# Performance work log

Measured on AMD Instinct MI355X. Metric: run time of the kernel, lower is better.

Reference implementation:

```python
import jax, jax.numpy as jnp
import numpy as np
from functools import partial

K_NEIGHBOURS = 16
POS_SLICE = (0, 2)  # pos_indices = slice(0, 2)


def setup_inputs() -> dict:
    key = jax.random.key(0)
    ks = jax.random.split(key, 8)
    B, A, D, H = 512, 128, 32, 128
    obs = jax.random.normal(ks[0], (B, A, D), dtype=jnp.float32)
    # GCNConv params (glorot-ish scale) and output MLP
    W1 = jax.random.normal(ks[1], (D, H), dtype=jnp.float32) / np.sqrt(D)
    b1 = jnp.zeros((H,), dtype=jnp.float32)
    W2 = jax.random.normal(ks[2], (H, H), dtype=jnp.float32) / np.sqrt(H)
    b2 = jnp.zeros((H,), dtype=jnp.float32)
    Wout = jax.random.normal(ks[3], (H, 1), dtype=jnp.float32) / np.sqrt(H)
    bout = jnp.zeros((1,), dtype=jnp.float32)
    return {"agent_observations": obs, "W1": W1, "b1": b1, "W2": W2, "b2": b2,
            "Wout": Wout, "bout": bout}


def _build_knn_edges(obs):
    """Vectorized kNN graph construction (replaces per-batch python loop).
    Returns (row, col) of shape [B*A*k] with batch offsets applied.
    row = source node i, col = j-th nearest neighbour of i (self excluded)."""
    B, A, _ = obs.shape
    k = K_NEIGHBOURS
    pos = obs[:, :, POS_SLICE[0]:POS_SLICE[1]]  # [B, A, 2]
    diff = pos[:, :, None, :] - pos[:, None, :, :]  # [B, A, A, 2]
    dist = jnp.sqrt(jnp.sum(diff * diff, axis=-1))  # [B, A, A] (cdist p=2)
    # k+1 smallest distances (self at distance 0 is dropped)
    _, knn_idx = jax.lax.top_k(-dist, k + 1)  # [B, A, k+1]
    neighbor_idx = knn_idx[..., 1:]  # [B, A, k]
    offsets = (jnp.arange(B, dtype=jnp.int32) * A)[:, None, None]
    src = jnp.broadcast_to(jnp.arange(A, dtype=jnp.int32)[None, :, None], (B, A, k)) + offsets
    dst = neighbor_idx.astype(jnp.int32) + offsets
    return src.reshape(-1), dst.reshape(-1)


def _gcn_conv(x, row, col, deg_inv_sqrt, W, b, num_nodes):
    """PyG GCNConv: self-loops + symmetric normalization.
    out[c] = sum_{(r,c) in E} d[r]*d[c]*(xW)[r] + d[c]^2*(xW)[c] + b"""
    h = x @ W  # [N, H]
    norm = deg_inv_sqrt[row] * deg_inv_sqrt[col]  # [E]
    agg = jax.ops.segment_sum(norm[:, None] * h[row], col, num_segments=num_nodes)
    self_term = (deg_inv_sqrt * deg_inv_sqrt)[:, None] * h  # self-loop messages
    return agg + self_term + b


def reference(agent_observations, W1, b1, W2, b2, Wout, bout):
    obs = agent_observations.astype(jnp.float32)
    B, A, D = obs.shape
    N = B * A
    row, col = _build_knn_edges(obs)
    x = obs.reshape(N, D)
    # degree with self-loop weight 1 (PyG gcn_norm): deg[c] = 1 + in-degree(c)
    deg = 1.0 + jax.ops.segment_sum(jnp.ones_like(col, dtype=x.dtype), col, num_segments=N)
    deg_inv_sqrt = jax.lax.rsqrt(deg)
    x = jnp.tanh(_gcn_conv(x, row, col, deg_inv_sqrt, W1, b1, N))
    x = jnp.tanh(_gcn_conv(x, row, col, deg_inv_sqrt, W2, b2, N))
    out = x @ Wout + bout  # [N, 1]
    return out.reshape(B, A, 1)
```

## Files before the change

kernel.cpp:

```cpp
#include <hip/hip_runtime.h>

#define NA 128
#define NKN 16

typedef _Float16 f16;
typedef __fp16   h16x2 __attribute__((ext_vector_type(2)));
typedef _Float16 f16x8 __attribute__((ext_vector_type(8)));
typedef float    f32x16 __attribute__((ext_vector_type(16)));
typedef unsigned long long u64;

#define MFMA __builtin_amdgcn_mfma_f32_32x32x16_f16
#define SWZ16(row, byteoff) ((byteoff) ^ (((row)&15)<<4))
#define SWZ4(row, byteoff)  ((byteoff) ^ (((row)&3)<<4))
#define CSW(ia, l) ((l) ^ (((ia) & 15) << 1))

__device__ __forceinline__ float tanh_fast(float x){
    float e = __expf(2.f * x);
    return 1.f - 2.f * __builtin_amdgcn_rcpf(e + 1.f);
}

__device__ __forceinline__ unsigned int wsel(const uint4 c, int i){
    return i==0 ? c.x : i==1 ? c.y : i==2 ? c.z : c.w;
}

__device__ __forceinline__ void agg_mm(const unsigned char* matIn, unsigned char* matOut,
                                       const unsigned int (*cmask)[4], const float* dinv_s,
                                       const float* bias, const u64* lut,
                                       int wv, int lane)
{
    const int lr = lane & 31, lg = lane >> 5;
    const int rb = wv & 3, ch = wv >> 2;
    f32x16 c0, c1;
    #pragma unroll
    for (int e = 0; e < 16; ++e) { c0[e] = 0.f; c1[e] = 0.f; }

    const int j0 = ch*64 + lr, j1 = j0 + 32;
    const uint4 cm0 = *(const uint4*)&cmask[j0][0];
    const uint4 cm1 = *(const uint4*)&cmask[j1][0];
    const int row = rb*32 + lr;

    #pragma unroll
    for (int ks = 0; ks < 8; ++ks) {
        f16x8 af = *(const f16x8*)(matIn + row*256 + SWZ16(row, ks*32 + lg*16));
        const int sh = (ks&1)*16 + lg*8;
        const unsigned int b0 = (wsel(cm0, ks>>1) >> sh) & 0xFFu;
        const unsigned int b1 = (wsel(cm1, ks>>1) >> sh) & 0xFFu;
        union { f16x8 v; u64 u[2]; } B0, B1;
        B0.u[0] = lut[b0 & 15u]; B0.u[1] = lut[b0 >> 4];
        B1.u[0] = lut[b1 & 15u]; B1.u[1] = lut[b1 >> 4];
        c0 = MFMA(af, B0.v, c0, 0, 0, 0);
        c1 = MFMA(af, B1.v, c1, 0, 0, 0);
    }
    #pragma unroll
    for (int ct = 0; ct < 2; ++ct) {
        const int j = ct ? j1 : j0;
        const float dj = dinv_s[j];
        #pragma unroll
        for (int q = 0; q < 4; ++q) {
            const int r0 = rb*32 + q*8 + lg*4;
            const float4 bv = *(const float4*)&bias[r0];
            float v0, v1, v2, v3;
            if (ct == 0) {
                v0 = tanh_fast(fmaf(dj, c0[q*4+0], bv.x));
                v1 = tanh_fast(fmaf(dj, c0[q*4+1], bv.y));
                v2 = tanh_fast(fmaf(dj, c0[q*4+2], bv.z));
                v3 = tanh_fast(fmaf(dj, c0[q*4+3], bv.w));
            } else {
                v0 = tanh_fast(fmaf(dj, c1[q*4+0], bv.x));
                v1 = tanh_fast(fmaf(dj, c1[q*4+1], bv.y));
                v2 = tanh_fast(fmaf(dj, c1[q*4+2], bv.z));
                v3 = tanh_fast(fmaf(dj, c1[q*4+3], bv.w));
            }
            union { h16x2 h[2]; u64 u; } pk;
            pk.h[0] = __builtin_amdgcn_cvt_pkrtz(v0, v1);
            pk.h[1] = __builtin_amdgcn_cvt_pkrtz(v2, v3);
            *(u64*)(matOut + j*256 + SWZ16(j, r0*2)) = pk.u;
        }
    }
}

__global__ __launch_bounds__(512, 1) void prep(const float* __restrict__ W1g,
                                               const float* __restrict__ W2g,
                                               unsigned char* __restrict__ ws)
{
    const int m = blockIdx.x * 512 + threadIdx.x;
    if (m < 2048) {
        const int h2 = m & 127, g = m >> 7;
        f16x8 v;
        #pragma unroll
        for (int s = 0; s < 8; ++s) v[s] = (f16)W2g[(g*8 + s)*128 + h2];
        *(f16x8*)(ws + 8192 + h2*256 + SWZ16(h2, g*16)) = v;
    } else {
        const int m2 = m - 2048;
        const int h = m2 & 127, g = m2 >> 7;
        f16x8 v;
        #pragma unroll
        for (int s = 0; s < 8; ++s) v[s] = (f16)W1g[(g*8 + s)*128 + h];
        *(f16x8*)(ws + h*64 + SWZ4(h, g*16)) = v;
    }
}

__global__ __launch_bounds__(512, 4) void gnn_fused(
    const float* __restrict__ obs,
    const unsigned char* __restrict__ ws,
    const float* __restrict__ b1g, const float* __restrict__ b2g,
    const float* __restrict__ Wog, const float* __restrict__ bog,
    float* __restrict__ outg)
{
    __shared__ __align__(16) unsigned char mat0[32768];
    __shared__ __align__(16) unsigned char mat1[32768];
    __shared__ float posx[NA], posy[NA], dinv_s[NA], b1s[NA], b2s[NA], wos[NA];
    __shared__ unsigned int cmask[NA][4];
    __shared__ unsigned int ccnt[NA];
    __shared__ u64 lut16[16];

    const int t = threadIdx.x;
    const int b = blockIdx.x;
    const int wv = t >> 6, lane = t & 63;
    const int lr = lane & 31, lg = lane >> 5;

    {
        const float4* ob = (const float4*)(obs + (size_t)b * NA * 32);
        #pragma unroll
        for (int rep = 0; rep < 2; ++rep) {
            const int idx = rep*512 + t;
            const int i = idx >> 3, seg = idx & 7;
            const float4 v = ob[idx];
            if (seg == 0) { posx[i] = v.x; posy[i] = v.y; }
            union { h16x2 h[2]; u64 u; } pk;
            pk.h[0] = __builtin_amdgcn_cvt_pkrtz(v.x, v.y);
            pk.h[1] = __builtin_amdgcn_cvt_pkrtz(v.z, v.w);
            *(u64*)(mat1 + i*64 + SWZ4(i, seg*8)) = pk.u;
        }
        u64* cand = (u64*)mat0;
        #pragma unroll
        for (int s = 0; s < 8; ++s) cand[t*8 + s] = ~0ull;
        if (t < NA) { b1s[t] = b1g[t]; b2s[t] = b2g[t]; wos[t] = Wog[t]; ccnt[t] = 0u; }
        { const int j = t >> 2, w = t & 3; cmask[j][w] = (w == (j>>5)) ? (1u << (j&31)) : 0u; }
        if (t < 16) {
            u64 e = 0ull;
            #pragma unroll
            for (int s = 0; s < 4; ++s)
                if ((t >> s) & 1) e |= 0x3C00ull << (16*s);
            lut16[t] = e;
        }
    }
    __syncthreads();

    const int ia = t >> 2, p4 = t & 3;
    {
        u64* cand = (u64*)mat0;
        unsigned int kd[32];
        const float xi = posx[ia], yi = posy[ia];
        #pragma unroll
        for (int jj = 0; jj < 32; ++jj) {
            const int j = p4*32 + jj;
            const float dx = __fsub_rn(xi, posx[j]);
            const float dy = __fsub_rn(yi, posy[j]);
            const float d  = __fsqrt_rn(__fadd_rn(__fmul_rn(dx,dx), __fmul_rn(dy,dy)));
            kd[jj] = __float_as_uint(d);
        }
        unsigned int lo = 0u, hi = 0xFF000000u, P = 0u;
        bool done = false;
        #pragma unroll 1
        for (int it = 0; it < 34; ++it) {
            const unsigned int mid = (lo + hi) >> 1;
            int cl = 0;
            #pragma unroll
            for (int jj = 0; jj < 32; ++jj) cl += (kd[jj] < mid) ? 1 : 0;
            cl += __shfl_xor(cl, 1, 64);
            cl += __shfl_xor(cl, 2, 64);
            if (!done) {
                if (cl >= 17 && cl <= 32) { P = mid; done = true; }
                else if (cl < 17) lo = mid;
                else hi = mid;
                if (hi - lo <= 1u && !done) { P = hi; done = true; }
            }
            if (__all(done ? 1 : 0)) break;
        }
        if (!done) P = hi;
        #pragma unroll
        for (int jj = 0; jj < 32; ++jj) {
            if (kd[jj] < P) {
                const unsigned int s = atomicAdd(&ccnt[ia], 1u);
                if (s < 32u)
                    cand[ia*32 + CSW(ia, s)] = ((u64)kd[jj] << 32) | (unsigned)(p4*32 + jj);
            }
        }
    }
    __syncthreads();
    {
        const u64* cand = (const u64*)mat0;
        u64 ck8[8];
        int rk[8];
        #pragma unroll
        for (int q = 0; q < 8; ++q) {
            ck8[q] = cand[ia*32 + CSW(ia, 8*p4 + q)];
            rk[q] = 0;
        }
        #pragma unroll
        for (int e = 0; e < 32; ++e) {
            const u64 ke = cand[ia*32 + CSW(ia, e)];
            #pragma unroll
            for (int q = 0; q < 8; ++q) rk[q] += (ke < ck8[q]) ? 1 : 0;
        }
        const int m = (int)min(ccnt[ia], 32u);
        #pragma unroll
        for (int q = 0; q < 8; ++q) {
            const int c = 8*p4 + q;
            if (c < m && rk[q] >= 1 && rk[q] < 17) {
                const int n = (int)(ck8[q] & 127u);
                atomicOr(&cmask[n][ia >> 5], 1u << (ia & 31));
            }
        }
    }
    __syncthreads();
    if (t < NA)
        dinv_s[t] = rsqrtf((float)(__popc(cmask[t][0]) + __popc(cmask[t][1]) +
                                   __popc(cmask[t][2]) + __popc(cmask[t][3])));
    *(f16x8*)(mat0 + t*16) = *(const f16x8*)(ws + t*16);
    __syncthreads();

    {
        f32x16 c0, c1;
        #pragma unroll
        for (int e = 0; e < 16; ++e) { c0[e] = 0.f; c1[e] = 0.f; }
        const int rb = wv & 3, ch = wv >> 2;
        const int row = rb*32 + lr;
        #pragma unroll
        for (int ks = 0; ks < 2; ++ks) {
            const f16x8 af = *(const f16x8*)(mat1 + row*64 + SWZ4(row, ks*32 + lg*16));
            #pragma unroll
            for (int ct = 0; ct < 2; ++ct) {
                const int h = ch*64 + ct*32 + lr;
                const f16x8 bf = *(const f16x8*)(mat0 + h*64 + SWZ4(h, ks*32 + lg*16));
                if (ct == 0) c0 = MFMA(af, bf, c0, 0, 0, 0);
                else         c1 = MFMA(af, bf, c1, 0, 0, 0);
            }
        }
        __syncthreads();
        #pragma unroll
        for (int ct = 0; ct < 2; ++ct) {
            const int h = ch*64 + ct*32 + lr;
            #pragma unroll
            for (int q = 0; q < 4; ++q) {
                const int r0 = rb*32 + q*8 + lg*4;
                const float4 dv = *(const float4*)&dinv_s[r0];
                union { h16x2 hh[2]; u64 u; } pk;
                if (ct == 0) {
                    pk.hh[0] = __builtin_amdgcn_cvt_pkrtz(c0[q*4+0]*dv.x, c0[q*4+1]*dv.y);
                    pk.hh[1] = __builtin_amdgcn_cvt_pkrtz(c0[q*4+2]*dv.z, c0[q*4+3]*dv.w);
                } else {
                    pk.hh[0] = __builtin_amdgcn_cvt_pkrtz(c1[q*4+0]*dv.x, c1[q*4+1]*dv.y);
                    pk.hh[1] = __builtin_amdgcn_cvt_pkrtz(c1[q*4+2]*dv.z, c1[q*4+3]*dv.w);
                }
                *(u64*)(mat0 + h*256 + SWZ16(h, r0*2)) = pk.u;
            }
        }
    }
    __syncthreads();

    agg_mm(mat0, mat1, cmask, dinv_s, b1s, lut16, wv, lane);
    __syncthreads();

    {
        #pragma unroll
        for (int rep = 0; rep < 4; ++rep) {
            const int idx = rep*512 + t;
            *(f16x8*)(mat0 + idx*16) = *(const f16x8*)(ws + 8192 + idx*16);
        }
    }
    __syncthreads();
    {
        f32x16 c0, c1;
        #pragma unroll
        for (int e = 0; e < 16; ++e) { c0[e] = 0.f; c1[e] = 0.f; }
        const int rb = wv & 3, ch = wv >> 2;
        const int row = rb*32 + lr;
        #pragma unroll
        for (int ks = 0; ks < 8; ++ks) {
            const f16x8 af = *(const f16x8*)(mat1 + row*256 + SWZ16(row, ks*32 + lg*16));
            #pragma unroll
            for (int ct = 0; ct < 2; ++ct) {
                const int h2 = ch*64 + ct*32 + lr;
                const f16x8 bf = *(const f16x8*)(mat0 + h2*256 + SWZ16(h2, ks*32 + lg*16));
                if (ct == 0) c0 = MFMA(af, bf, c0, 0, 0, 0);
                else         c1 = MFMA(af, bf, c1, 0, 0, 0);
            }
        }
        __syncthreads();
        #pragma unroll
        for (int ct = 0; ct < 2; ++ct) {
            const int h2 = ch*64 + ct*32 + lr;
            #pragma unroll
            for (int q = 0; q < 4; ++q) {
                const int r0 = rb*32 + q*8 + lg*4;
                const float4 dv = *(const float4*)&dinv_s[r0];
                union { h16x2 hh[2]; u64 u; } pk;
                if (ct == 0) {
                    pk.hh[0] = __builtin_amdgcn_cvt_pkrtz(c0[q*4+0]*dv.x, c0[q*4+1]*dv.y);
                    pk.hh[1] = __builtin_amdgcn_cvt_pkrtz(c0[q*4+2]*dv.z, c0[q*4+3]*dv.w);
                } else {
                    pk.hh[0] = __builtin_amdgcn_cvt_pkrtz(c1[q*4+0]*dv.x, c1[q*4+1]*dv.y);
                    pk.hh[1] = __builtin_amdgcn_cvt_pkrtz(c1[q*4+2]*dv.z, c1[q*4+3]*dv.w);
                }
                *(u64*)(mat1 + h2*256 + SWZ16(h2, r0*2)) = pk.u;
            }
        }
    }
    __syncthreads();

    agg_mm(mat1, mat0, cmask, dinv_s, b2s, lut16, wv, lane);
    __syncthreads();

    {
        float s = 0.f;
        #pragma unroll
        for (int u = 0; u < 4; ++u) {
            const f16x8 v = *(const f16x8*)(mat0 + ia*256 + SWZ16(ia, p4*64 + u*16));
            const float4 w0 = *(const float4*)&wos[p4*32 + u*8];
            const float4 w1 = *(const float4*)&wos[p4*32 + u*8 + 4];
            s = fmaf((float)v[0], w0.x, s); s = fmaf((float)v[1], w0.y, s);
            s = fmaf((float)v[2], w0.z, s); s = fmaf((float)v[3], w0.w, s);
            s = fmaf((float)v[4], w1.x, s); s = fmaf((float)v[5], w1.y, s);
            s = fmaf((float)v[6], w1.z, s); s = fmaf((float)v[7], w1.w, s);
        }
        s += __shfl_xor(s, 1, 64);
        s += __shfl_xor(s, 2, 64);
        if (p4 == 0) outg[b*NA + ia] = s + bog[0];
    }
}

extern "C" void kernel_launch(void* const* d_in, const int* in_sizes, int n_in,
                              void* d_out, int out_size, void* d_ws, size_t ws_size,
                              hipStream_t stream) {
    const float* obs = (const float*)d_in[0];
    const float* W1  = (const float*)d_in[1];
    const float* b1  = (const float*)d_in[2];
    const float* W2  = (const float*)d_in[3];
    const float* b2  = (const float*)d_in[4];
    const float* Wo  = (const float*)d_in[5];
    const float* bo  = (const float*)d_in[6];
    float* out = (float*)d_out;
    const int B = in_sizes[0] / (NA * 32);
    unsigned char* ws = (unsigned char*)d_ws;
    hipLaunchKernelGGL(prep, dim3(5), dim3(512), 0, stream, W1, W2, ws);
    hipLaunchKernelGGL(gnn_fused, dim3(B), dim3(512), 0, stream,
                       obs, ws, b1, b2, Wo, bo, out);
}
```

Measured before the change: 37.98 us.

## Double block size to 1024 threads, each wave computing one 32x32 tile

The fused GNN kernel now launches 1024 threads (16 waves) per batch element instead of 512. Each wave owns a single 32x32 output tile in the matmul and aggregation stages instead of two, and each node's kNN work is split across 8 threads instead of 4. The aim is more waves per CU and shorter per-thread serial chains, to hide latency better. In exchange there are more barrier participants, more shuffles in the reductions, and LDS use per block limits how many blocks fit on a CU.

```diff
diff --git a/kernel.cpp b/kernel.cpp
--- a/kernel.cpp
+++ b/kernel.cpp
@@ -29,53 +29,37 @@
                                        int wv, int lane)
 {
     const int lr = lane & 31, lg = lane >> 5;
-    const int rb = wv & 3, ch = wv >> 2;
-    f32x16 c0, c1;
+    const int rb = wv & 3, cb = wv >> 2;
+    f32x16 c0;
     #pragma unroll
-    for (int e = 0; e < 16; ++e) { c0[e] = 0.f; c1[e] = 0.f; }
-
-    const int j0 = ch*64 + lr, j1 = j0 + 32;
-    const uint4 cm0 = *(const uint4*)&cmask[j0][0];
-    const uint4 cm1 = *(const uint4*)&cmask[j1][0];
+    for (int e = 0; e < 16; ++e) c0[e] = 0.f;
+
+    const int j = cb*32 + lr;
+    const uint4 cm = *(const uint4*)&cmask[j][0];
     const int row = rb*32 + lr;
 
     #pragma unroll
     for (int ks = 0; ks < 8; ++ks) {
         f16x8 af = *(const f16x8*)(matIn + row*256 + SWZ16(row, ks*32 + lg*16));
         const int sh = (ks&1)*16 + lg*8;
-        const unsigned int b0 = (wsel(cm0, ks>>1) >> sh) & 0xFFu;
-        const unsigned int b1 = (wsel(cm1, ks>>1) >> sh) & 0xFFu;
-        union { f16x8 v; u64 u[2]; } B0, B1;
-        B0.u[0] = lut[b0 & 15u]; B0.u[1] = lut[b0 >> 4];
-        B1.u[0] = lut[b1 & 15u]; B1.u[1] = lut[b1 >> 4];
+        const unsigned int bb = (wsel(cm, ks>>1) >> sh) & 0xFFu;
+        union { f16x8 v; u64 u[2]; } B0;
+        B0.u[0] = lut[bb & 15u]; B0.u[1] = lut[bb >> 4];
         c0 = MFMA(af, B0.v, c0, 0, 0, 0);
-        c1 = MFMA(af, B1.v, c1, 0, 0, 0);
-    }
+    }
+    const float dj = dinv_s[j];
     #pragma unroll
-    for (int ct = 0; ct < 2; ++ct) {
-        const int j = ct ? j1 : j0;
-        const float dj = dinv_s[j];
-        #pragma unroll
-        for (int q = 0; q < 4; ++q) {
-            const int r0 = rb*32 + q*8 + lg*4;
-            const float4 bv = *(const float4*)&bias[r0];
-            float v0, v1, v2, v3;
-            if (ct == 0) {
-                v0 = tanh_fast(fmaf(dj, c0[q*4+0], bv.x));
-                v1 = tanh_fast(fmaf(dj, c0[q*4+1], bv.y));
-                v2 = tanh_fast(fmaf(dj, c0[q*4+2], bv.z));
-                v3 = tanh_fast(fmaf(dj, c0[q*4+3], bv.w));
-            } else {
-                v0 = tanh_fast(fmaf(dj, c1[q*4+0], bv.x));
-                v1 = tanh_fast(fmaf(dj, c1[q*4+1], bv.y));
-                v2 = tanh_fast(fmaf(dj, c1[q*4+2], bv.z));
-                v3 = tanh_fast(fmaf(dj, c1[q*4+3], bv.w));
-            }
-            union { h16x2 h[2]; u64 u; } pk;
-            pk.h[0] = __builtin_amdgcn_cvt_pkrtz(v0, v1);
-            pk.h[1] = __builtin_amdgcn_cvt_pkrtz(v2, v3);
-            *(u64*)(matOut + j*256 + SWZ16(j, r0*2)) = pk.u;
-        }
+    for (int q = 0; q < 4; ++q) {
+        const int r0 = rb*32 + q*8 + lg*4;
+        const float4 bv = *(const float4*)&bias[r0];
+        const float v0 = tanh_fast(fmaf(dj, c0[q*4+0], bv.x));
+        const float v1 = tanh_fast(fmaf(dj, c0[q*4+1], bv.y));
+        const float v2 = tanh_fast(fmaf(dj, c0[q*4+2], bv.z));
+        const float v3 = tanh_fast(fmaf(dj, c0[q*4+3], bv.w));
+        union { h16x2 h[2]; u64 u; } pk;
+        pk.h[0] = __builtin_amdgcn_cvt_pkrtz(v0, v1);
+        pk.h[1] = __builtin_amdgcn_cvt_pkrtz(v2, v3);
+        *(u64*)(matOut + j*256 + SWZ16(j, r0*2)) = pk.u;
     }
 }
 
@@ -100,7 +84,7 @@
     }
 }
 
-__global__ __launch_bounds__(512, 4) void gnn_fused(
+__global__ __launch_bounds__(1024, 8) void gnn_fused(
     const float* __restrict__ obs,
     const unsigned char* __restrict__ ws,
     const float* __restrict__ b1g, const float* __restrict__ b2g,
@@ -121,11 +105,9 @@
 
     {
         const float4* ob = (const float4*)(obs + (size_t)b * NA * 32);
-        #pragma unroll
-        for (int rep = 0; rep < 2; ++rep) {
-            const int idx = rep*512 + t;
-            const int i = idx >> 3, seg = idx & 7;
-            const float4 v = ob[idx];
+        {
+            const int i = t >> 3, seg = t & 7;
+            const float4 v = ob[t];
             if (seg == 0) { posx[i] = v.x; posy[i] = v.y; }
             union { h16x2 h[2]; u64 u; } pk;
             pk.h[0] = __builtin_amdgcn_cvt_pkrtz(v.x, v.y);
@@ -134,9 +116,9 @@
         }
         u64* cand = (u64*)mat0;
         #pragma unroll
-        for (int s = 0; s < 8; ++s) cand[t*8 + s] = ~0ull;
+        for (int s = 0; s < 4; ++s) cand[t*4 + s] = ~0ull;
         if (t < NA) { b1s[t] = b1g[t]; b2s[t] = b2g[t]; wos[t] = Wog[t]; ccnt[t] = 0u; }
-        { const int j = t >> 2, w = t & 3; cmask[j][w] = (w == (j>>5)) ? (1u << (j&31)) : 0u; }
+        if (t < 512) { const int j = t >> 2, w = t & 3; cmask[j][w] = (w == (j>>5)) ? (1u << (j&31)) : 0u; }
         if (t < 16) {
             u64 e = 0ull;
             #pragma unroll
@@ -147,14 +129,14 @@
     }
     __syncthreads();
 
-    const int ia = t >> 2, p4 = t & 3;
+    const int ia = t >> 3, p8 = t & 7;
     {
         u64* cand = (u64*)mat0;
-        unsigned int kd[32];
+        unsigned int kd[16];
         const float xi = posx[ia], yi = posy[ia];
         #pragma unroll
-        for (int jj = 0; jj < 32; ++jj) {
-            const int j = p4*32 + jj;
+        for (int jj = 0; jj < 16; ++jj) {
+            const int j = p8*16 + jj;
             const float dx = __fsub_rn(xi, posx[j]);
             const float dy = __fsub_rn(yi, posy[j]);
             const float d  = __fsqrt_rn(__fadd_rn(__fmul_rn(dx,dx), __fmul_rn(dy,dy)));
@@ -167,9 +149,10 @@
             const unsigned int mid = (lo + hi) >> 1;
             int cl = 0;
             #pragma unroll
-            for (int jj = 0; jj < 32; ++jj) cl += (kd[jj] < mid) ? 1 : 0;
+            for (int jj = 0; jj < 16; ++jj) cl += (kd[jj] < mid) ? 1 : 0;
             cl += __shfl_xor(cl, 1, 64);
             cl += __shfl_xor(cl, 2, 64);
+            cl += __shfl_xor(cl, 4, 64);
             if (!done) {
                 if (cl >= 17 && cl <= 32) { P = mid; done = true; }
                 else if (cl < 17) lo = mid;
@@ -180,36 +163,36 @@
         }
         if (!done) P = hi;
         #pragma unroll
-        for (int jj = 0; jj < 32; ++jj) {
+        for (int jj = 0; jj < 16; ++jj) {
             if (kd[jj] < P) {
                 const unsigned int s = atomicAdd(&ccnt[ia], 1u);
                 if (s < 32u)
-                    cand[ia*32 + CSW(ia, s)] = ((u64)kd[jj] << 32) | (unsigned)(p4*32 + jj);
+                    cand[ia*32 + CSW(ia, s)] = ((u64)kd[jj] << 32) | (unsigned)(p8*16 + jj);
             }
         }
     }
     __syncthreads();
     {
         const u64* cand = (const u64*)mat0;
-        u64 ck8[8];
-        int rk[8];
-        #pragma unroll
-        for (int q = 0; q < 8; ++q) {
-            ck8[q] = cand[ia*32 + CSW(ia, 8*p4 + q)];
+        u64 ck4[4];
+        int rk[4];
+        #pragma unroll
+        for (int q = 0; q < 4; ++q) {
+            ck4[q] = cand[ia*32 + CSW(ia, 4*p8 + q)];
             rk[q] = 0;
         }
         #pragma unroll
         for (int e = 0; e < 32; ++e) {
             const u64 ke = cand[ia*32 + CSW(ia, e)];
             #pragma unroll
-            for (int q = 0; q < 8; ++q) rk[q] += (ke < ck8[q]) ? 1 : 0;
+            for (int q = 0; q < 4; ++q) rk[q] += (ke < ck4[q]) ? 1 : 0;
         }
         const int m = (int)min(ccnt[ia], 32u);
         #pragma unroll
-        for (int q = 0; q < 8; ++q) {
-            const int c = 8*p4 + q;
+        for (int q = 0; q < 4; ++q) {
+            const int c = 4*p8 + q;
             if (c < m && rk[q] >= 1 && rk[q] < 17) {
-                const int n = (int)(ck8[q] & 127u);
+                const int n = (int)(ck4[q] & 127u);
                 atomicOr(&cmask[n][ia >> 5], 1u << (ia & 31));
             }
         }
@@ -218,44 +201,31 @@
     if (t < NA)
         dinv_s[t] = rsqrtf((float)(__popc(cmask[t][0]) + __popc(cmask[t][1]) +
                                    __popc(cmask[t][2]) + __popc(cmask[t][3])));
-    *(f16x8*)(mat0 + t*16) = *(const f16x8*)(ws + t*16);
-    __syncthreads();
-
-    {
-        f32x16 c0, c1;
-        #pragma unroll
-        for (int e = 0; e < 16; ++e) { c0[e] = 0.f; c1[e] = 0.f; }
-        const int rb = wv & 3, ch = wv >> 2;
+    if (t < 512) *(f16x8*)(mat0 + t*16) = *(const f16x8*)(ws + t*16);
+    __syncthreads();
+
+    {
+        f32x16 c0;
+        #pragma unroll
+        for (int e = 0; e < 16; ++e) c0[e] = 0.f;
+        const int rb = wv & 3, cb = wv >> 2;
         const int row = rb*32 + lr;
+        const int h = cb*32 + lr;
         #pragma unroll
         for (int ks = 0; ks < 2; ++ks) {
             const f16x8 af = *(const f16x8*)(mat1 + row*64 + SWZ4(row, ks*32 + lg*16));
-            #pragma unroll
-            for (int ct = 0; ct < 2; ++ct) {
-                const int h = ch*64 + ct*32 + lr;
-                const f16x8 bf = *(const f16x8*)(mat0 + h*64 + SWZ4(h, ks*32 + lg*16));
-                if (ct == 0) c0 = MFMA(af, bf, c0, 0, 0, 0);
-                else         c1 = MFMA(af, bf, c1, 0, 0, 0);
-            }
+            const f16x8 bf = *(const f16x8*)(mat0 + h*64 + SWZ4(h, ks*32 + lg*16));
+            c0 = MFMA(af, bf, c0, 0, 0, 0);
         }
         __syncthreads();
         #pragma unroll
-        for (int ct = 0; ct < 2; ++ct) {
-            const int h = ch*64 + ct*32 + lr;
-            #pragma unroll
-            for (int q = 0; q < 4; ++q) {
-                const int r0 = rb*32 + q*8 + lg*4;
-                const float4 dv = *(const float4*)&dinv_s[r0];
-                union { h16x2 hh[2]; u64 u; } pk;
-                if (ct == 0) {
-                    pk.hh[0] = __builtin_amdgcn_cvt_pkrtz(c0[q*4+0]*dv.x, c0[q*4+1]*dv.y);
-                    pk.hh[1] = __builtin_amdgcn_cvt_pkrtz(c0[q*4+2]*dv.z, c0[q*4+3]*dv.w);
-                } else {
-                    pk.hh[0] = __builtin_amdgcn_cvt_pkrtz(c1[q*4+0]*dv.x, c1[q*4+1]*dv.y);
-                    pk.hh[1] = __builtin_amdgcn_cvt_pkrtz(c1[q*4+2]*dv.z, c1[q*4+3]*dv.w);
-                }
-                *(u64*)(mat0 + h*256 + SWZ16(h, r0*2)) = pk.u;
-            }
+        for (int q = 0; q < 4; ++q) {
+            const int r0 = rb*32 + q*8 + lg*4;
+            const float4 dv = *(const float4*)&dinv_s[r0];
+            union { h16x2 hh[2]; u64 u; } pk;
+            pk.hh[0] = __builtin_amdgcn_cvt_pkrtz(c0[q*4+0]*dv.x, c0[q*4+1]*dv.y);
+            pk.hh[1] = __builtin_amdgcn_cvt_pkrtz(c0[q*4+2]*dv.z, c0[q*4+3]*dv.w);
+            *(u64*)(mat0 + h*256 + SWZ16(h, r0*2)) = pk.u;
         }
     }
     __syncthreads();
@@ -265,47 +235,34 @@
 
     {
         #pragma unroll
-        for (int rep = 0; rep < 4; ++rep) {
-            const int idx = rep*512 + t;
+        for (int rep = 0; rep < 2; ++rep) {
+            const int idx = rep*1024 + t;
             *(f16x8*)(mat0 + idx*16) = *(const f16x8*)(ws + 8192 + idx*16);
         }
     }
     __syncthreads();
     {
-        f32x16 c0, c1;
-        #pragma unroll
-        for (int e = 0; e < 16; ++e) { c0[e] = 0.f; c1[e] = 0.f; }
-        const int rb = wv & 3, ch = wv >> 2;
+        f32x16 c0;
+        #pragma unroll
+        for (int e = 0; e < 16; ++e) c0[e] = 0.f;
+        const int rb = wv & 3, cb = wv >> 2;
         const int row = rb*32 + lr;
+        const int h2 = cb*32 + lr;
         #pragma unroll
         for (int ks = 0; ks < 8; ++ks) {
             const f16x8 af = *(const f16x8*)(mat1 + row*256 + SWZ16(row, ks*32 + lg*16));
-            #pragma unroll
-            for (int ct = 0; ct < 2; ++ct) {
-                const int h2 = ch*64 + ct*32 + lr;
-                const f16x8 bf = *(const f16x8*)(mat0 + h2*256 + SWZ16(h2, ks*32 + lg*16));
-                if (ct == 0) c0 = MFMA(af, bf, c0, 0, 0, 0);
-                else         c1 = MFMA(af, bf, c1, 0, 0, 0);
-            }
+            const f16x8 bf = *(const f16x8*)(mat0 + h2*256 + SWZ16(h2, ks*32 + lg*16));
+            c0 = MFMA(af, bf, c0, 0, 0, 0);
         }
         __syncthreads();
         #pragma unroll
-        for (int ct = 0; ct < 2; ++ct) {
-            const int h2 = ch*64 + ct*32 + lr;
-            #pragma unroll
-            for (int q = 0; q < 4; ++q) {
-                const int r0 = rb*32 + q*8 + lg*4;
-                const float4 dv = *(const float4*)&dinv_s[r0];
-                union { h16x2 hh[2]; u64 u; } pk;
-                if (ct == 0) {
-                    pk.hh[0] = __builtin_amdgcn_cvt_pkrtz(c0[q*4+0]*dv.x, c0[q*4+1]*dv.y);
-                    pk.hh[1] = __builtin_amdgcn_cvt_pkrtz(c0[q*4+2]*dv.z, c0[q*4+3]*dv.w);
-                } else {
-                    pk.hh[0] = __builtin_amdgcn_cvt_pkrtz(c1[q*4+0]*dv.x, c1[q*4+1]*dv.y);
-                    pk.hh[1] = __builtin_amdgcn_cvt_pkrtz(c1[q*4+2]*dv.z, c1[q*4+3]*dv.w);
-                }
-                *(u64*)(mat1 + h2*256 + SWZ16(h2, r0*2)) = pk.u;
-            }
+        for (int q = 0; q < 4; ++q) {
+            const int r0 = rb*32 + q*8 + lg*4;
+            const float4 dv = *(const float4*)&dinv_s[r0];
+            union { h16x2 hh[2]; u64 u; } pk;
+            pk.hh[0] = __builtin_amdgcn_cvt_pkrtz(c0[q*4+0]*dv.x, c0[q*4+1]*dv.y);
+            pk.hh[1] = __builtin_amdgcn_cvt_pkrtz(c0[q*4+2]*dv.z, c0[q*4+3]*dv.w);
+            *(u64*)(mat1 + h2*256 + SWZ16(h2, r0*2)) = pk.u;
         }
     }
     __syncthreads();
@@ -316,10 +273,10 @@
     {
         float s = 0.f;
         #pragma unroll
-        for (int u = 0; u < 4; ++u) {
-            const f16x8 v = *(const f16x8*)(mat0 + ia*256 + SWZ16(ia, p4*64 + u*16));
-            const float4 w0 = *(const float4*)&wos[p4*32 + u*8];
-            const float4 w1 = *(const float4*)&wos[p4*32 + u*8 + 4];
+        for (int u = 0; u < 2; ++u) {
+            const f16x8 v = *(const f16x8*)(mat0 + ia*256 + SWZ16(ia, p8*32 + u*16));
+            const float4 w0 = *(const float4*)&wos[p8*16 + u*8];
+            const float4 w1 = *(const float4*)&wos[p8*16 + u*8 + 4];
             s = fmaf((float)v[0], w0.x, s); s = fmaf((float)v[1], w0.y, s);
             s = fmaf((float)v[2], w0.z, s); s = fmaf((float)v[3], w0.w, s);
             s = fmaf((float)v[4], w1.x, s); s = fmaf((float)v[5], w1.y, s);
@@ -327,7 +284,8 @@
         }
         s += __shfl_xor(s, 1, 64);
         s += __shfl_xor(s, 2, 64);
-        if (p4 == 0) outg[b*NA + ia] = s + bog[0];
+        s += __shfl_xor(s, 4, 64);
+        if (p8 == 0) outg[b*NA + ia] = s + bog[0];
     }
 }
 
@@ -345,6 +303,6 @@
     const int B = in_sizes[0] / (NA * 32);
     unsigned char* ws = (unsigned char*)d_ws;
     hipLaunchKernelGGL(prep, dim3(5), dim3(512), 0, stream, W1, W2, ws);
-    hipLaunchKernelGGL(gnn_fused, dim3(B), dim3(512), 0, stream,
+    hipLaunchKernelGGL(gnn_fused, dim3(B), dim3(1024), 0, stream,
                        obs, ws, b1, b2, Wo, bo, out);
 }
```

New measurement: 56.97 us. 50.0% more time.
